# Optimization experiments

Measured on AMD Instinct MI355X. Metric: run time of the kernel, lower is better.

Reference implementation:

```python
import jax, jax.numpy as jnp
import numpy as np

N = 50000
E = 640000
IN_DIM = 23
HID = 128
NUM_CLASS = 12


def setup_inputs() -> dict:
    key = jax.random.key(0)
    ks = jax.random.split(key, 12)
    x = jax.random.normal(ks[0], (N, IN_DIM), dtype=jnp.float32)
    edge_index = jax.random.randint(ks[1], (2, E), 0, N, dtype=jnp.int32)

    def glorot(k, shape):
        fan_in, fan_out = shape
        lim = np.sqrt(6.0 / (fan_in + fan_out)).astype(np.float32)
        return jax.random.uniform(k, shape, jnp.float32, -lim, lim)

    W1 = glorot(ks[2], (IN_DIM, HID)); b1 = jnp.zeros((HID,), jnp.float32)
    W2 = glorot(ks[3], (HID, HID));    b2 = jnp.zeros((HID,), jnp.float32)
    W3 = glorot(ks[4], (HID, HID));    b3 = jnp.zeros((HID,), jnp.float32)
    Wc1 = glorot(ks[5], (HID, 64));    bc1 = jnp.zeros((64,), jnp.float32)
    Wc2 = glorot(ks[6], (64, NUM_CLASS)); bc2 = jnp.zeros((NUM_CLASS,), jnp.float32)
    return {"x": x, "edge_index": edge_index,
            "W1": W1, "b1": b1, "W2": W2, "b2": b2, "W3": W3, "b3": b3,
            "Wc1": Wc1, "bc1": bc1, "Wc2": Wc2, "bc2": bc2}


def _gcn_norm(edge_index, n_nodes):
    # add self loops, compute symmetric normalization D^-1/2 (A+I) D^-1/2
    loop = jnp.arange(n_nodes, dtype=edge_index.dtype)
    src = jnp.concatenate([edge_index[0], loop])
    dst = jnp.concatenate([edge_index[1], loop])
    deg = jax.ops.segment_sum(jnp.ones_like(dst, dtype=jnp.float32), dst,
                              num_segments=n_nodes)
    dinv = jax.lax.rsqrt(deg)  # deg >= 1 due to self loops
    norm = dinv[src] * dinv[dst]  # [E + N]
    return src, dst, norm


def _gcn_layer(h, W, b, src, dst, norm, n_nodes):
    h = h @ W                          # linear (bias applied after aggregation, per PyG)
    msg = h[src] * norm[:, None]       # gather + scale
    out = jax.ops.segment_sum(msg, dst, num_segments=n_nodes)  # scatter-add
    return out + b


def reference(x, edge_index, W1, b1, W2, b2, W3, b3, Wc1, bc1, Wc2, bc2):
    n = x.shape[0]
    src, dst, norm = _gcn_norm(edge_index, n)
    h = jnp.tanh(_gcn_layer(x, W1, b1, src, dst, norm, n))
    h = jnp.tanh(_gcn_layer(h, W2, b2, src, dst, norm, n))
    h = jnp.tanh(_gcn_layer(h, W3, b3, src, dst, norm, n))
    # dropout is identity in eval mode
    out = h @ Wc1 + bc1
    out = out @ Wc2 + bc2
    return out
```

## Files before the change

### kernel.cpp

```cpp
#include <hip/hip_runtime.h>
#include <math.h>

#define NN 50000
#define EE 640000
#define IND 23
#define HID 128
#define MIDD 64
#define NCLS 12
#define NB 49
#define QS 32766.0f
#define INVQS (1.0f / 32766.0f)

typedef short short8v __attribute__((ext_vector_type(8)));


__global__ void k_count(const int* __restrict__ dst, int* __restrict__ cnt, int e) {
    int i = blockIdx.x * blockDim.x + threadIdx.x;
    if (i < e) atomicAdd(&cnt[dst[i]], 1);
}

__global__ __launch_bounds__(256) void k_scan_local(const int* __restrict__ cnt,
                                                    int* __restrict__ row_ptr,
                                                    float* __restrict__ dinv,
                                                    int* __restrict__ sums) {
    __shared__ int wtot[4];
    const int tid = threadIdx.x;
    const int wid = tid >> 6, lane = tid & 63;
    const int base = blockIdx.x * 1024 + tid * 4;
    int v[4];
#pragma unroll
    for (int t = 0; t < 4; ++t) {
        int i = base + t;
        v[t] = (i < NN) ? cnt[i] : 0;
        if (i < NN) dinv[i] = rsqrtf((float)v[t] + 1.0f);
    }
    int slocal = v[0] + v[1] + v[2] + v[3];
    int val = slocal;
#pragma unroll
    for (int off = 1; off < 64; off <<= 1) {
        int t = __shfl_up(val, off, 64);
        if (lane >= off) val += t;
    }
    if (lane == 63) wtot[wid] = val;
    __syncthreads();
    int woff = 0;
#pragma unroll
    for (int w = 0; w < 4; ++w) woff += (w < wid) ? wtot[w] : 0;
    int run = woff + val - slocal;
#pragma unroll
    for (int t = 0; t < 4; ++t) {
        int i = base + t;
        if (i < NN) row_ptr[i] = run;
        run += v[t];
    }
    if (tid == 255) sums[blockIdx.x] = woff + val;
}

__global__ void k_scan_sums(const int* __restrict__ sums, int* __restrict__ offs,
                            int* __restrict__ row_ptr) {
    const int lane = threadIdx.x;
    int v = (lane < NB) ? sums[lane] : 0;
    int val = v;
#pragma unroll
    for (int off = 1; off < 64; off <<= 1) {
        int t = __shfl_up(val, off, 64);
        if (lane >= off) val += t;
    }
    if (lane < NB) offs[lane] = val - v;
    if (lane == NB - 1) row_ptr[NN] = val;
}

__global__ __launch_bounds__(256) void k_scan_apply(int* __restrict__ row_ptr,
                                                    const int* __restrict__ offs,
                                                    int* __restrict__ cursor) {
    const int base = blockIdx.x * 1024 + threadIdx.x * 4;
    const int o = offs[blockIdx.x];
#pragma unroll
    for (int t = 0; t < 4; ++t) {
        int i = base + t;
        if (i < NN) {
            int rp = row_ptr[i] + o;
            row_ptr[i] = rp;
            cursor[i] = rp;
        }
    }
}

__global__ void k_fill(const int* __restrict__ src, const int* __restrict__ dst,
                       int* __restrict__ cursor, int* __restrict__ e_src, int e) {
    int i = blockIdx.x * blockDim.x + threadIdx.x;
    if (i < e) {
        int d = dst[i];
        int pos = atomicAdd(&cursor[d], 1);
        e_src[pos] = src[i];
    }
}

__global__ __launch_bounds__(256) void k_pad(const float* __restrict__ x,
                                             const float* __restrict__ dinv,
                                             float* __restrict__ xp) {
    int i = blockIdx.x * 256 + threadIdx.x;
    int node = i >> 5, f = i & 31;
    xp[i] = (f < IND) ? x[node * IND + f] * dinv[node] : 0.f;
}

__global__ __launch_bounds__(256) void k_l1(const float* __restrict__ xp,
                                            const float* __restrict__ W1,
                                            const float* __restrict__ b1,
                                            const int* __restrict__ row_ptr,
                                            const int* __restrict__ e_src,
                                            const float* __restrict__ dinv,
                                            short* __restrict__ outq) {
    const int tid = threadIdx.x;
    const int i = blockIdx.x * 4 + (tid >> 6);
    const int lane = tid & 63;
    const int slot = lane >> 3;
    const int f = lane & 7;
    const float4* xp4 = (const float4*)xp;
    const int beg = row_ptr[i];
    const int deg = row_ptr[i + 1] - beg;
    float4 acc = make_float4(0.f, 0.f, 0.f, 0.f);
    for (int base = 0; base < deg; base += 64) {
        const int cnt = min(64, deg - base);
        int s_l = 0;
        if (lane < cnt) s_l = e_src[beg + base + lane];
        int e = 0;
        for (; e + 8 <= cnt; e += 8) {
            int s = __shfl(s_l, e + slot, 64);
            float4 v = xp4[s * 8 + f];
            acc.x += v.x; acc.y += v.y; acc.z += v.z; acc.w += v.w;
        }
        if (e < cnt) {
            int s = __shfl(s_l, e + slot, 64);
            if (e + slot < cnt) {
                float4 v = xp4[s * 8 + f];
                acc.x += v.x; acc.y += v.y; acc.z += v.z; acc.w += v.w;
            }
        }
    }
#pragma unroll
    for (int off = 32; off >= 8; off >>= 1) {
        acc.x += __shfl_down(acc.x, off, 64);
        acc.y += __shfl_down(acc.y, off, 64);
        acc.z += __shfl_down(acc.z, off, 64);
        acc.w += __shfl_down(acc.w, off, 64);
    }
    const float di = dinv[i];
    if (lane < 8) {
        float4 v = xp4[i * 8 + lane];
        acc.x = (acc.x + v.x) * di; acc.y = (acc.y + v.y) * di;
        acc.z = (acc.z + v.z) * di; acc.w = (acc.w + v.w) * di;
    }
    float a0 = b1[lane], a1 = b1[lane + 64];
#pragma unroll
    for (int k = 0; k < IND; ++k) {
        float comp = ((k & 3) == 0) ? acc.x : ((k & 3) == 1) ? acc.y
                   : ((k & 3) == 2) ? acc.z : acc.w;
        float xk = __shfl(comp, k >> 2, 64);
        a0 += xk * W1[k * HID + lane];
        a1 += xk * W1[k * HID + lane + 64];
    }
    outq[i * HID + lane]      = (short)__float2int_rn(tanhf(a0) * QS);
    outq[i * HID + lane + 64] = (short)__float2int_rn(tanhf(a1) * QS);
}

__global__ __launch_bounds__(256) void k_aggq(const short* __restrict__ hq,
                                              const int* __restrict__ row_ptr,
                                              const int* __restrict__ e_src,
                                              const float* __restrict__ dinv,
                                              float* __restrict__ aggf) {
    const int tid = threadIdx.x;
    const int i = blockIdx.x * 4 + (tid >> 6);
    const int lane = tid & 63;
    const int slot = lane >> 4;
    const int f = lane & 15;
    const short8v* h8 = (const short8v*)hq;
    const int beg = row_ptr[i];
    const int deg = row_ptr[i + 1] - beg;
    float facc[8];
#pragma unroll
    for (int t = 0; t < 8; ++t) facc[t] = 0.f;
    for (int base = 0; base < deg; base += 64) {
        const int cnt = min(64, deg - base);
        int s_l = 0; float n_l = 0.f;
        if (lane < cnt) {
            s_l = e_src[beg + base + lane];
            n_l = dinv[s_l];
        }
        int e = 0;
#pragma unroll 2
        for (; e + 4 <= cnt; e += 4) {
            int s = __shfl(s_l, e + slot, 64);
            float nr = __shfl(n_l, e + slot, 64);
            short8v v = h8[s * 16 + f];
#pragma unroll
            for (int t = 0; t < 8; ++t) facc[t] += (float)v[t] * nr;
        }
        if (e < cnt) {
            int s = __shfl(s_l, e + slot, 64);
            float nr = __shfl(n_l, e + slot, 64);
            if (e + slot < cnt) {
                short8v v = h8[s * 16 + f];
#pragma unroll
                for (int t = 0; t < 8; ++t) facc[t] += (float)v[t] * nr;
            }
        }
    }
#pragma unroll
    for (int off = 32; off >= 16; off >>= 1)
#pragma unroll
        for (int t = 0; t < 8; ++t) facc[t] += __shfl_down(facc[t], off, 64);
    if (lane < 16) {
        const float di = dinv[i];
        const float sc = di * INVQS;
        short8v v = h8[i * 16 + lane];
        float4 o0, o1;
        o0.x = (facc[0] + di * (float)v[0]) * sc;
        o0.y = (facc[1] + di * (float)v[1]) * sc;
        o0.z = (facc[2] + di * (float)v[2]) * sc;
        o0.w = (facc[3] + di * (float)v[3]) * sc;
        o1.x = (facc[4] + di * (float)v[4]) * sc;
        o1.y = (facc[5] + di * (float)v[5]) * sc;
        o1.z = (facc[6] + di * (float)v[6]) * sc;
        o1.w = (facc[7] + di * (float)v[7]) * sc;
        ((float4*)aggf)[i * 32 + lane * 2]     = o0;
        ((float4*)aggf)[i * 32 + lane * 2 + 1] = o1;
    }
}

__global__ __launch_bounds__(256) void k_gemmT(const float* __restrict__ hin,
                                               const float* __restrict__ W,
                                               const float* __restrict__ bias,
                                               short* __restrict__ qout,
                                               float* __restrict__ fout) {
    __shared__ float Hs[64 * 36];
    __shared__ float Ws[32 * 128];
    const int tid = threadIdx.x;
    const int b0 = blockIdx.x * 64;
    const int ng = tid >> 4;
    const int cg = tid & 15;
    const float4* hin4 = (const float4*)hin;
    const float4* W4 = (const float4*)W;

    float acc[4][8];
#pragma unroll
    for (int m = 0; m < 4; ++m)
#pragma unroll
        for (int c = 0; c < 8; ++c) acc[m][c] = 0.f;

    for (int ks = 0; ks < HID; ks += 32) {
#pragma unroll
        for (int t = 0; t < 2; ++t) {
            int id = t * 256 + tid;
            int row = id >> 3;
            int k4 = id & 7;
            int node = b0 + row;
            float4 v = make_float4(0.f, 0.f, 0.f, 0.f);
            if (node < NN) v = hin4[node * 32 + (ks >> 2) + k4];
            *(float4*)&Hs[row * 36 + k4 * 4] = v;
        }
#pragma unroll
        for (int t = 0; t < 4; ++t) {
            int id = t * 256 + tid;
            int row = id >> 5;
            int c4 = id & 31;
            *(float4*)&Ws[row * 128 + c4 * 4] = W4[(ks + row) * 32 + c4];
        }
        __syncthreads();
#pragma unroll 8
        for (int kk = 0; kk < 32; ++kk) {
            float4 w0 = *(float4*)&Ws[kk * 128 + cg * 8];
            float4 w1 = *(float4*)&Ws[kk * 128 + cg * 8 + 4];
#pragma unroll
            for (int m = 0; m < 4; ++m) {
                float hv = Hs[(ng * 4 + m) * 36 + kk];
                acc[m][0] += hv * w0.x; acc[m][1] += hv * w0.y;
                acc[m][2] += hv * w0.z; acc[m][3] += hv * w0.w;
                acc[m][4] += hv * w1.x; acc[m][5] += hv * w1.y;
                acc[m][6] += hv * w1.z; acc[m][7] += hv * w1.w;
            }
        }
        __syncthreads();
    }
    const float4* b4 = (const float4*)bias;
    float4 bb0 = b4[cg * 2], bb1 = b4[cg * 2 + 1];
#pragma unroll
    for (int m = 0; m < 4; ++m) {
        int node = b0 + ng * 4 + m;
        if (node < NN) {
            float t0 = tanhf(acc[m][0] + bb0.x);
            float t1 = tanhf(acc[m][1] + bb0.y);
            float t2 = tanhf(acc[m][2] + bb0.z);
            float t3 = tanhf(acc[m][3] + bb0.w);
            float t4 = tanhf(acc[m][4] + bb1.x);
            float t5 = tanhf(acc[m][5] + bb1.y);
            float t6 = tanhf(acc[m][6] + bb1.z);
            float t7 = tanhf(acc[m][7] + bb1.w);
            if (qout) {
                short8v qv;
                qv[0] = (short)__float2int_rn(t0 * QS);
                qv[1] = (short)__float2int_rn(t1 * QS);
                qv[2] = (short)__float2int_rn(t2 * QS);
                qv[3] = (short)__float2int_rn(t3 * QS);
                qv[4] = (short)__float2int_rn(t4 * QS);
                qv[5] = (short)__float2int_rn(t5 * QS);
                qv[6] = (short)__float2int_rn(t6 * QS);
                qv[7] = (short)__float2int_rn(t7 * QS);
                ((short8v*)qout)[node * 16 + cg] = qv;
            }
            if (fout) {
                ((float4*)fout)[node * 32 + cg * 2]     = make_float4(t0, t1, t2, t3);
                ((float4*)fout)[node * 32 + cg * 2 + 1] = make_float4(t4, t5, t6, t7);
            }
        }
    }
}


__global__ __launch_bounds__(256) void k_cls(const float* __restrict__ h,
                                             const float* __restrict__ Wc1,
                                             const float* __restrict__ bc1,
                                             const float* __restrict__ Wc2,
                                             const float* __restrict__ bc2,
                                             float* __restrict__ out) {
    __shared__ float hs[16 * 128];
    __shared__ float ms[16 * 65];
    const int tid = threadIdx.x;
    const int b0 = blockIdx.x * 16;
    const float4* h4 = (const float4*)h;
#pragma unroll
    for (int t = 0; t < 2; ++t) {
        int id = t * 256 + tid;
        int node = id >> 5;
        int k4 = id & 31;
        float4 v = make_float4(0.f, 0.f, 0.f, 0.f);
        if (b0 + node < NN) v = h4[(b0 + node) * 32 + k4];
        *(float4*)&hs[node * 128 + k4 * 4] = v;
    }
    __syncthreads();
    const int q = tid >> 6;
    const int c = tid & 63;
    float acc[4];
#pragma unroll
    for (int t = 0; t < 4; ++t) acc[t] = 0.f;
    for (int k = 0; k < HID; ++k) {
        float w = Wc1[k * MIDD + c];
#pragma unroll
        for (int t = 0; t < 4; ++t) acc[t] += hs[(q + 4 * t) * 128 + k] * w;
    }
    float bb = bc1[c];
#pragma unroll
    for (int t = 0; t < 4; ++t) ms[(q + 4 * t) * 65 + c] = acc[t] + bb;
    __syncthreads();
    if (tid < 16 * NCLS) {
        int m = tid / NCLS;
        int cls = tid % NCLS;
        int node = b0 + m;
        if (node < NN) {
            float o = bc2[cls];
#pragma unroll 8
            for (int k = 0; k < MIDD; ++k) o += ms[m * 65 + k] * Wc2[k * NCLS + cls];
            out[node * NCLS + cls] = o;
        }
    }
}


extern "C" void kernel_launch(void* const* d_in, const int* in_sizes, int n_in,
                              void* d_out, int out_size, void* d_ws, size_t ws_size,
                              hipStream_t stream) {
    const float* x    = (const float*)d_in[0];
    const int*   edge = (const int*)d_in[1];
    const int*   src  = edge;
    const int*   dst  = edge + EE;
    const float* W1  = (const float*)d_in[2];  const float* b1  = (const float*)d_in[3];
    const float* W2  = (const float*)d_in[4];  const float* b2  = (const float*)d_in[5];
    const float* W3  = (const float*)d_in[6];  const float* b3  = (const float*)d_in[7];
    const float* Wc1 = (const float*)d_in[8];  const float* bc1 = (const float*)d_in[9];
    const float* Wc2 = (const float*)d_in[10]; const float* bc2 = (const float*)d_in[11];
    float* outp = (float*)d_out;

    char* p = (char*)d_ws;
    int*   cnt     = (int*)p;   p += 200064;
    int*   row_ptr = (int*)p;   p += 200064;
    float* dinv    = (float*)p; p += 200064;
    int*   sums    = (int*)p;   p += 256;
    int*   offs    = (int*)p;   p += 256;
    int*   e_src   = (int*)p;   p += (size_t)EE * 4;
    float* xp      = (float*)p; p += (size_t)NN * 32 * 4;
    short* q       = (short*)p; p += (size_t)NN * HID * 2;
    float* aggf    = (float*)p; p += (size_t)NN * HID * 4;

    hipMemsetAsync(cnt, 0, (size_t)NN * 4, stream);
    k_count     <<<(EE + 255) / 256, 256, 0, stream>>>(dst, cnt, EE);
    k_scan_local<<<NB, 256, 0, stream>>>(cnt, row_ptr, dinv, sums);
    k_scan_sums <<<1, 64, 0, stream>>>(sums, offs, row_ptr);
    k_scan_apply<<<NB, 256, 0, stream>>>(row_ptr, offs, cnt);
    k_fill      <<<(EE + 255) / 256, 256, 0, stream>>>(src, dst, cnt, e_src, EE);
    k_pad       <<<(NN * 32) / 256, 256, 0, stream>>>(x, dinv, xp);

    k_l1  <<<NN / 4, 256, 0, stream>>>(xp, W1, b1, row_ptr, e_src, dinv, q);
    k_aggq <<<NN / 4, 256, 0, stream>>>(q, row_ptr, e_src, dinv, aggf);
    k_gemmT<<<(NN + 63) / 64, 256, 0, stream>>>(aggf, W2, b2, q, nullptr);
    k_aggq <<<NN / 4, 256, 0, stream>>>(q, row_ptr, e_src, dinv, aggf);
    k_gemmT<<<(NN + 63) / 64, 256, 0, stream>>>(aggf, W3, b3, nullptr, aggf);
    k_cls<<<(NN + 15) / 16, 256, 0, stream>>>(aggf, Wc1, bc1, Wc2, bc2, outp);
}
```

Before: 341.2 us.

## Fuse aggregation, GEMM, tanh and classifier into per-layer kernels

Merges the gather-aggregation, the dense 128x128 transform with tanh, and (for the last layer) the two classifier matmuls into one kernel per layer. Aggregated rows go into a 64-row shared-memory tile instead of a global fp32 buffer. This removes the global write and re-read of the float aggregation, and the float hidden state before the classifier. Layer outputs now ping-pong between two short buffers. In exchange, each block of 4 waves aggregates 16 nodes serially per wave. The large shared tile (about 50 KB) may limit occupancy for the latency-bound gather phase.

Measured after the change: 445.1 us. +30.4%, slower.

```diff
diff --git a/kernel.cpp b/kernel.cpp
--- a/kernel.cpp
+++ b/kernel.cpp
@@ -164,84 +164,96 @@
     outq[i * HID + lane + 64] = (short)__float2int_rn(tanhf(a1) * QS);
 }
 
-__global__ __launch_bounds__(256) void k_aggq(const short* __restrict__ hq,
-                                              const int* __restrict__ row_ptr,
-                                              const int* __restrict__ e_src,
-                                              const float* __restrict__ dinv,
-                                              float* __restrict__ aggf) {
+template <bool LAST>
+__global__ __launch_bounds__(256) void k_layer(const short* __restrict__ qin,
+                                               const float* __restrict__ W,
+                                               const float* __restrict__ bias,
+                                               const int* __restrict__ row_ptr,
+                                               const int* __restrict__ e_src,
+                                               const float* __restrict__ dinv,
+                                               short* __restrict__ qout,
+                                               const float* __restrict__ Wc1,
+                                               const float* __restrict__ bc1,
+                                               const float* __restrict__ Wc2,
+                                               const float* __restrict__ bc2,
+                                               float* __restrict__ outp) {
+    __shared__ float Hs[64 * 132];
+    __shared__ float Ws[4160];
     const int tid = threadIdx.x;
-    const int i = blockIdx.x * 4 + (tid >> 6);
+    const int b0 = blockIdx.x * 64;
+    const int wv = tid >> 6;
     const int lane = tid & 63;
     const int slot = lane >> 4;
     const int f = lane & 15;
-    const short8v* h8 = (const short8v*)hq;
-    const int beg = row_ptr[i];
-    const int deg = row_ptr[i + 1] - beg;
-    float facc[8];
-#pragma unroll
-    for (int t = 0; t < 8; ++t) facc[t] = 0.f;
-    for (int base = 0; base < deg; base += 64) {
-        const int cnt = min(64, deg - base);
-        int s_l = 0; float n_l = 0.f;
-        if (lane < cnt) {
-            s_l = e_src[beg + base + lane];
-            n_l = dinv[s_l];
-        }
-        int e = 0;
+    const short8v* h8 = (const short8v*)qin;
+
+    for (int t = 0; t < 16; ++t) {
+        const int row = wv * 16 + t;
+        const int i = b0 + row;
+        if (i < NN) {
+            const int beg = row_ptr[i];
+            const int deg = row_ptr[i + 1] - beg;
+            float facc[8];
+#pragma unroll
+            for (int c = 0; c < 8; ++c) facc[c] = 0.f;
+            for (int base = 0; base < deg; base += 64) {
+                const int cnt = min(64, deg - base);
+                int s_l = 0; float n_l = 0.f;
+                if (lane < cnt) {
+                    s_l = e_src[beg + base + lane];
+                    n_l = dinv[s_l];
+                }
+                int e = 0;
 #pragma unroll 2
-        for (; e + 4 <= cnt; e += 4) {
-            int s = __shfl(s_l, e + slot, 64);
-            float nr = __shfl(n_l, e + slot, 64);
-            short8v v = h8[s * 16 + f];
-#pragma unroll
-            for (int t = 0; t < 8; ++t) facc[t] += (float)v[t] * nr;
-        }
-        if (e < cnt) {
-            int s = __shfl(s_l, e + slot, 64);
-            float nr = __shfl(n_l, e + slot, 64);
-            if (e + slot < cnt) {
-                short8v v = h8[s * 16 + f];
-#pragma unroll
-                for (int t = 0; t < 8; ++t) facc[t] += (float)v[t] * nr;
-            }
-        }
-    }
-#pragma unroll
-    for (int off = 32; off >= 16; off >>= 1)
-#pragma unroll
-        for (int t = 0; t < 8; ++t) facc[t] += __shfl_down(facc[t], off, 64);
-    if (lane < 16) {
-        const float di = dinv[i];
-        const float sc = di * INVQS;
-        short8v v = h8[i * 16 + lane];
-        float4 o0, o1;
-        o0.x = (facc[0] + di * (float)v[0]) * sc;
-        o0.y = (facc[1] + di * (float)v[1]) * sc;
-        o0.z = (facc[2] + di * (float)v[2]) * sc;
-        o0.w = (facc[3] + di * (float)v[3]) * sc;
-        o1.x = (facc[4] + di * (float)v[4]) * sc;
-        o1.y = (facc[5] + di * (float)v[5]) * sc;
-        o1.z = (facc[6] + di * (float)v[6]) * sc;
-        o1.w = (facc[7] + di * (float)v[7]) * sc;
-        ((float4*)aggf)[i * 32 + lane * 2]     = o0;
-        ((float4*)aggf)[i * 32 + lane * 2 + 1] = o1;
-    }
-}
-
-__global__ __launch_bounds__(256) void k_gemmT(const float* __restrict__ hin,
-                                               const float* __restrict__ W,
-                                               const float* __restrict__ bias,
-                                               short* __restrict__ qout,
-                                               float* __restrict__ fout) {
-    __shared__ float Hs[64 * 36];
-    __shared__ float Ws[32 * 128];
-    const int tid = threadIdx.x;
-    const int b0 = blockIdx.x * 64;
+                for (; e + 4 <= cnt; e += 4) {
+                    int s = __shfl(s_l, e + slot, 64);
+                    float nr = __shfl(n_l, e + slot, 64);
+                    short8v v = h8[s * 16 + f];
+#pragma unroll
+                    for (int c = 0; c < 8; ++c) facc[c] += (float)v[c] * nr;
+                }
+                if (e < cnt) {
+                    int s = __shfl(s_l, e + slot, 64);
+                    float nr = __shfl(n_l, e + slot, 64);
+                    if (e + slot < cnt) {
+                        short8v v = h8[s * 16 + f];
+#pragma unroll
+                        for (int c = 0; c < 8; ++c) facc[c] += (float)v[c] * nr;
+                    }
+                }
+            }
+#pragma unroll
+            for (int off = 32; off >= 16; off >>= 1)
+#pragma unroll
+                for (int c = 0; c < 8; ++c) facc[c] += __shfl_down(facc[c], off, 64);
+            if (lane < 16) {
+                const float di = dinv[i];
+                const float sc = di * INVQS;
+                short8v v = h8[i * 16 + lane];
+                float* dstp = &Hs[row * 132 + lane * 8];
+                float4 o0, o1;
+                o0.x = (facc[0] + di * (float)v[0]) * sc;
+                o0.y = (facc[1] + di * (float)v[1]) * sc;
+                o0.z = (facc[2] + di * (float)v[2]) * sc;
+                o0.w = (facc[3] + di * (float)v[3]) * sc;
+                o1.x = (facc[4] + di * (float)v[4]) * sc;
+                o1.y = (facc[5] + di * (float)v[5]) * sc;
+                o1.z = (facc[6] + di * (float)v[6]) * sc;
+                o1.w = (facc[7] + di * (float)v[7]) * sc;
+                *(float4*)dstp = o0;
+                *(float4*)(dstp + 4) = o1;
+            }
+        } else if (lane < 16) {
+            float* dstp = &Hs[row * 132 + lane * 8];
+            *(float4*)dstp = make_float4(0.f, 0.f, 0.f, 0.f);
+            *(float4*)(dstp + 4) = make_float4(0.f, 0.f, 0.f, 0.f);
+        }
+    }
+    __syncthreads();
+
     const int ng = tid >> 4;
     const int cg = tid & 15;
-    const float4* hin4 = (const float4*)hin;
     const float4* W4 = (const float4*)W;
-
     float acc[4][8];
 #pragma unroll
     for (int m = 0; m < 4; ++m)
@@ -249,16 +261,6 @@
         for (int c = 0; c < 8; ++c) acc[m][c] = 0.f;
 
     for (int ks = 0; ks < HID; ks += 32) {
-#pragma unroll
-        for (int t = 0; t < 2; ++t) {
-            int id = t * 256 + tid;
-            int row = id >> 3;
-            int k4 = id & 7;
-            int node = b0 + row;
-            float4 v = make_float4(0.f, 0.f, 0.f, 0.f);
-            if (node < NN) v = hin4[node * 32 + (ks >> 2) + k4];
-            *(float4*)&Hs[row * 36 + k4 * 4] = v;
-        }
 #pragma unroll
         for (int t = 0; t < 4; ++t) {
             int id = t * 256 + tid;
@@ -273,7 +275,7 @@
             float4 w1 = *(float4*)&Ws[kk * 128 + cg * 8 + 4];
 #pragma unroll
             for (int m = 0; m < 4; ++m) {
-                float hv = Hs[(ng * 4 + m) * 36 + kk];
+                float hv = Hs[(ng * 4 + m) * 132 + ks + kk];
                 acc[m][0] += hv * w0.x; acc[m][1] += hv * w0.y;
                 acc[m][2] += hv * w0.z; acc[m][3] += hv * w0.w;
                 acc[m][4] += hv * w1.x; acc[m][5] += hv * w1.y;
@@ -286,17 +288,18 @@
     float4 bb0 = b4[cg * 2], bb1 = b4[cg * 2 + 1];
 #pragma unroll
     for (int m = 0; m < 4; ++m) {
-        int node = b0 + ng * 4 + m;
-        if (node < NN) {
-            float t0 = tanhf(acc[m][0] + bb0.x);
-            float t1 = tanhf(acc[m][1] + bb0.y);
-            float t2 = tanhf(acc[m][2] + bb0.z);
-            float t3 = tanhf(acc[m][3] + bb0.w);
-            float t4 = tanhf(acc[m][4] + bb1.x);
-            float t5 = tanhf(acc[m][5] + bb1.y);
-            float t6 = tanhf(acc[m][6] + bb1.z);
-            float t7 = tanhf(acc[m][7] + bb1.w);
-            if (qout) {
+        int row = ng * 4 + m;
+        int node = b0 + row;
+        float t0 = tanhf(acc[m][0] + bb0.x);
+        float t1 = tanhf(acc[m][1] + bb0.y);
+        float t2 = tanhf(acc[m][2] + bb0.z);
+        float t3 = tanhf(acc[m][3] + bb0.w);
+        float t4 = tanhf(acc[m][4] + bb1.x);
+        float t5 = tanhf(acc[m][5] + bb1.y);
+        float t6 = tanhf(acc[m][6] + bb1.z);
+        float t7 = tanhf(acc[m][7] + bb1.w);
+        if (!LAST) {
+            if (node < NN) {
                 short8v qv;
                 qv[0] = (short)__float2int_rn(t0 * QS);
                 qv[1] = (short)__float2int_rn(t1 * QS);
@@ -308,59 +311,41 @@
                 qv[7] = (short)__float2int_rn(t7 * QS);
                 ((short8v*)qout)[node * 16 + cg] = qv;
             }
-            if (fout) {
-                ((float4*)fout)[node * 32 + cg * 2]     = make_float4(t0, t1, t2, t3);
-                ((float4*)fout)[node * 32 + cg * 2 + 1] = make_float4(t4, t5, t6, t7);
-            }
-        }
-    }
-}
-
-
-__global__ __launch_bounds__(256) void k_cls(const float* __restrict__ h,
-                                             const float* __restrict__ Wc1,
-                                             const float* __restrict__ bc1,
-                                             const float* __restrict__ Wc2,
-                                             const float* __restrict__ bc2,
-                                             float* __restrict__ out) {
-    __shared__ float hs[16 * 128];
-    __shared__ float ms[16 * 65];
-    const int tid = threadIdx.x;
-    const int b0 = blockIdx.x * 16;
-    const float4* h4 = (const float4*)h;
-#pragma unroll
-    for (int t = 0; t < 2; ++t) {
-        int id = t * 256 + tid;
-        int node = id >> 5;
-        int k4 = id & 31;
-        float4 v = make_float4(0.f, 0.f, 0.f, 0.f);
-        if (b0 + node < NN) v = h4[(b0 + node) * 32 + k4];
-        *(float4*)&hs[node * 128 + k4 * 4] = v;
-    }
-    __syncthreads();
-    const int q = tid >> 6;
-    const int c = tid & 63;
-    float acc[4];
-#pragma unroll
-    for (int t = 0; t < 4; ++t) acc[t] = 0.f;
-    for (int k = 0; k < HID; ++k) {
-        float w = Wc1[k * MIDD + c];
-#pragma unroll
-        for (int t = 0; t < 4; ++t) acc[t] += hs[(q + 4 * t) * 128 + k] * w;
-    }
-    float bb = bc1[c];
-#pragma unroll
-    for (int t = 0; t < 4; ++t) ms[(q + 4 * t) * 65 + c] = acc[t] + bb;
-    __syncthreads();
-    if (tid < 16 * NCLS) {
-        int m = tid / NCLS;
-        int cls = tid % NCLS;
-        int node = b0 + m;
-        if (node < NN) {
-            float o = bc2[cls];
+        } else {
+            float* dstp = &Hs[row * 132 + cg * 8];
+            *(float4*)dstp = make_float4(t0, t1, t2, t3);
+            *(float4*)(dstp + 4) = make_float4(t4, t5, t6, t7);
+        }
+    }
+
+    if (LAST) {
+        __syncthreads();
+        const int c = tid & 63;
+        const int q4 = tid >> 6;
+        float a2[16];
+#pragma unroll
+        for (int t = 0; t < 16; ++t) a2[t] = 0.f;
+        for (int k = 0; k < HID; ++k) {
+            float w = Wc1[k * MIDD + c];
+#pragma unroll
+            for (int t = 0; t < 16; ++t) a2[t] += Hs[(q4 * 16 + t) * 132 + k] * w;
+        }
+        float bb = bc1[c];
+#pragma unroll
+        for (int t = 0; t < 16; ++t) Ws[(q4 * 16 + t) * 65 + c] = a2[t] + bb;
+        __syncthreads();
+#pragma unroll
+        for (int t = 0; t < 3; ++t) {
+            int idx = tid + 256 * t;
+            int m = idx / NCLS;
+            int cls = idx - m * NCLS;
+            int node = b0 + m;
+            if (node < NN) {
+                float o = bc2[cls];
 #pragma unroll 8
-            for (int k = 0; k < MIDD; ++k) o += ms[m * 65 + k] * Wc2[k * NCLS + cls];
-            out[node * NCLS + cls] = o;
+                for (int k = 0; k < MIDD; ++k) o += Ws[m * 65 + k] * Wc2[k * NCLS + cls];
+                outp[node * NCLS + cls] = o;
+            }
         }
     }
 }
@@ -388,8 +373,8 @@
     int*   offs    = (int*)p;   p += 256;
     int*   e_src   = (int*)p;   p += (size_t)EE * 4;
     float* xp      = (float*)p; p += (size_t)NN * 32 * 4;
-    short* q       = (short*)p; p += (size_t)NN * HID * 2;
-    float* aggf    = (float*)p; p += (size_t)NN * HID * 4;
+    short* q1      = (short*)p; p += (size_t)NN * HID * 2;
+    short* q2      = (short*)p; p += (size_t)NN * HID * 2;
 
     hipMemsetAsync(cnt, 0, (size_t)NN * 4, stream);
     k_count     <<<(EE + 255) / 256, 256, 0, stream>>>(dst, cnt, EE);
@@ -399,10 +384,11 @@
     k_fill      <<<(EE + 255) / 256, 256, 0, stream>>>(src, dst, cnt, e_src, EE);
     k_pad       <<<(NN * 32) / 256, 256, 0, stream>>>(x, dinv, xp);
 
-    k_l1  <<<NN / 4, 256, 0, stream>>>(xp, W1, b1, row_ptr, e_src, dinv, q);
-    k_aggq <<<NN / 4, 256, 0, stream>>>(q, row_ptr, e_src, dinv, aggf);
-    k_gemmT<<<(NN + 63) / 64, 256, 0, stream>>>(aggf, W2, b2, q, nullptr);
-    k_aggq <<<NN / 4, 256, 0, stream>>>(q, row_ptr, e_src, dinv, aggf);
-    k_gemmT<<<(NN + 63) / 64, 256, 0, stream>>>(aggf, W3, b3, nullptr, aggf);
-    k_cls<<<(NN + 15) / 16, 256, 0, stream>>>(aggf, Wc1, bc1, Wc2, bc2, outp);
-}
+    k_l1<<<NN / 4, 256, 0, stream>>>(xp, W1, b1, row_ptr, e_src, dinv, q1);
+    k_layer<false><<<(NN + 63) / 64, 256, 0, stream>>>(
+        q1, W2, b2, row_ptr, e_src, dinv, q2,
+        nullptr, nullptr, nullptr, nullptr, nullptr);
+    k_layer<true><<<(NN + 63) / 64, 256, 0, stream>>>(
+        q2, W3, b3, row_ptr, e_src, dinv, nullptr,
+        Wc1, bc1, Wc2, bc2, outp);
+}
```
